# Kernel tuning notes

Measured on AMD Instinct MI355X. Metric: run time of the kernel, lower is better.

The kernel has to match this reference:

```python
import jax, jax.numpy as jnp
import numpy as np

DIM = 256
HEADS = 8
NX = NY = 48
RNG = 5
MAX_IDX = (RNG + 1) ** 2  # 36, padding token


def _make_tokens(nx, ny, rng):
    # Half-symmetric tokenization of 2D relative positions (Learnable_rel_pos_embedding.tokenize)
    xm, ym = np.meshgrid(np.arange(nx), np.arange(ny), indexing='ij')
    xm, ym = xm.ravel(), ym.ravel()
    dx = xm[None, :] - xm[:, None]
    dy = ym[None, :] - ym[:, None]
    tok = np.abs(dx) * (rng + 1) + np.abs(dy)
    tok[(np.abs(dx) > rng) | (np.abs(dy) > rng)] = MAX_IDX
    return tok.astype(np.int32)


def setup_inputs() -> dict:
    key = jax.random.key(0)
    ks = jax.random.split(key, 10)
    s = DIM ** -0.5
    x = jax.random.normal(ks[0], (1, DIM, NX, NY), dtype=jnp.float32)
    Wq = jax.random.normal(ks[1], (DIM, DIM), dtype=jnp.float32) * s
    bq = jax.random.normal(ks[2], (DIM,), dtype=jnp.float32) * 0.01
    Wk = jax.random.normal(ks[3], (DIM, DIM), dtype=jnp.float32) * s
    bk = jax.random.normal(ks[4], (DIM,), dtype=jnp.float32) * 0.01
    Wv = jax.random.normal(ks[5], (DIM, DIM), dtype=jnp.float32) * s
    bv = jax.random.normal(ks[6], (DIM,), dtype=jnp.float32) * 0.01
    Wp = jax.random.normal(ks[7], (DIM, DIM), dtype=jnp.float32) * s
    bp = jax.random.normal(ks[8], (DIM,), dtype=jnp.float32) * 0.01
    emb = jax.random.normal(ks[9], (MAX_IDX + 1, HEADS), dtype=jnp.float32) * 0.02
    tokens = jnp.asarray(_make_tokens(NX, NY, RNG))  # (N, N) int32
    return dict(x=x, Wq=Wq, bq=bq, Wk=Wk, bk=bk, Wv=Wv, bv=bv,
                Wp=Wp, bp=bp, emb=emb, tokens=tokens)


def reference(x, Wq, bq, Wk, bk, Wv, bv, Wp, bp, emb, tokens):
    B, C, nx, ny = x.shape
    H = emb.shape[1]
    hd = C // H
    N = nx * ny
    scale = hd ** -0.5

    def conv1x1(W, b, t):
        return (jnp.einsum('oc,bcxy->boxy', W, t) + b[None, :, None, None])

    # Q/K/V as 1x1 convs, split into heads: (B, H, hd, N)
    q = conv1x1(Wq, bq, x).reshape(B, H, hd, N)
    k = conv1x1(Wk, bk, x).reshape(B, H, hd, N)
    v = conv1x1(Wv, bv, x).reshape(B, H, hd, N)

    # attn_method=2: scores = scale*QK^T + relative positional bias
    scores = jnp.einsum('bhdn,bhdm->bhnm', q, k) * scale  # (B, H, N, N)

    # pos_type=5: embedding lookup over half-symmetric relative-position tokens
    pad = emb.shape[0] - 1
    emb_masked = emb.at[pad].set(0.0)  # padding_idx row is zero
    pe = emb_masked[tokens]            # (N, N, H)
    scores = scores + jnp.transpose(pe, (2, 0, 1))[None]

    attn = jax.nn.softmax(scores, axis=-1)
    out = jnp.einsum('bhnm,bhdm->bhdn', attn, v).reshape(B, C, nx, ny)
    out = conv1x1(Wp, bp, out)
    return out
```

## Files before the change

### kernel.cpp

```cpp
#include <hip/hip_runtime.h>

#define NN 2304
#define CC 256
#define HH 8
#define HD 32
#define NYY 48
#define SCALE 0.17677669529663687f

typedef __bf16 bf16_t;
typedef __bf16 bf8v __attribute__((ext_vector_type(8)));
typedef __bf16 bf4v __attribute__((ext_vector_type(4)));
typedef float f4v __attribute__((ext_vector_type(4)));

__device__ __forceinline__ f4v mfma16(bf8v a, bf8v b, f4v c) {
    return __builtin_amdgcn_mfma_f32_16x16x32_bf16(a, b, c, 0, 0, 0);
}

__global__ __launch_bounds__(256) void k_pre(
    const float* __restrict__ x, bf16_t* __restrict__ xT,
    const float* __restrict__ Wq, const float* __restrict__ Wk,
    const float* __restrict__ Wv, const float* __restrict__ Wp,
    bf16_t* __restrict__ Wb) {
    const int b = blockIdx.x;
    const int t = threadIdx.x;
    if (b < 288) {
        __shared__ float tile[64][33];
        const int c0 = (b & 7) * 32;
        const int n0 = (b >> 3) * 64;
        const int n = t & 63, cb = t >> 6;
#pragma unroll
        for (int cc = 0; cc < 8; cc++) {
            int c = cc * 4 + cb;
            tile[n][c] = x[(size_t)(c0 + c) * NN + n0 + n];
        }
        __syncthreads();
        const int c = t & 31, nb = t >> 5;
#pragma unroll
        for (int nn = 0; nn < 8; nn++) {
            int n2 = nn * 8 + nb;
            xT[(size_t)(n0 + n2) * CC + c0 + c] = (bf16_t)tile[n2][c];
        }
    } else {
        const int wb = b - 288;
        const int matid = wb >> 5;
        const float* src = (matid == 0) ? Wq : (matid == 1) ? Wk : (matid == 2) ? Wv : Wp;
        const int base = (wb & 31) * 2048 + t * 8;
        float4 a = *(const float4*)(src + base);
        float4 c = *(const float4*)(src + base + 4);
        bf8v o;
        o[0] = (bf16_t)a.x; o[1] = (bf16_t)a.y; o[2] = (bf16_t)a.z; o[3] = (bf16_t)a.w;
        o[4] = (bf16_t)c.x; o[5] = (bf16_t)c.y; o[6] = (bf16_t)c.z; o[7] = (bf16_t)c.w;
        *(bf8v*)(Wb + (size_t)matid * 65536 + base) = o;
    }
}

__global__ __launch_bounds__(256) void k_proj_qkv(
    const bf16_t* __restrict__ Wb,
    const float* __restrict__ bq, const float* __restrict__ bk,
    const float* __restrict__ bv,
    const bf16_t* __restrict__ xT,
    bf16_t* __restrict__ Qt, bf16_t* __restrict__ Kt, bf16_t* __restrict__ Vd) {
    const int mat = blockIdx.z;
    const bf16_t* W = Wb + (size_t)mat * 65536;
    const float* bias = (mat == 0) ? bq : (mat == 1) ? bk : bv;
    const int n0 = blockIdx.x * 32;
    const int o0 = blockIdx.y * 64;
    const int lane = threadIdx.x & 63;
    const int wave = threadIdx.x >> 6;
    const int l15 = lane & 15;
    const int quad = lane >> 4;
    const int orow = o0 + wave * 16;

    f4v acc0 = {0.f, 0.f, 0.f, 0.f}, acc1 = {0.f, 0.f, 0.f, 0.f};
#pragma unroll
    for (int k0 = 0; k0 < CC; k0 += 32) {
        bf8v af = *(const bf8v*)(W + (size_t)(orow + l15) * CC + k0 + quad * 8);
        bf8v b0 = *(const bf8v*)(xT + (size_t)(n0 + l15) * CC + k0 + quad * 8);
        bf8v b1 = *(const bf8v*)(xT + (size_t)(n0 + 16 + l15) * CC + k0 + quad * 8);
        acc0 = mfma16(af, b0, acc0);
        acc1 = mfma16(af, b1, acc1);
    }

#pragma unroll
    for (int r = 0; r < 4; r++) {
        const int o = orow + quad * 4 + r;
        const float bo = bias[o];
#pragma unroll
        for (int nb = 0; nb < 2; nb++) {
            const int n = n0 + nb * 16 + l15;
            float v = (nb ? acc1[r] : acc0[r]) + bo;
            if (mat == 2) {
                Vd[(size_t)o * NN + n] = (bf16_t)v;
            } else {
                int h = o >> 5, d = o & 31;
                bf16_t* dst = (mat == 0) ? Qt : Kt;
                float vv = (mat == 0) ? v * SCALE : v;
                dst[(size_t)h * NN * HD + (size_t)n * HD + d] = (bf16_t)vv;
            }
        }
    }
}

template <int NITER, int S>
__global__ __launch_bounds__(256, 6) void k_attn_split(
    const bf16_t* __restrict__ Qt, const bf16_t* __restrict__ Kt,
    const bf16_t* __restrict__ Vd, const float* __restrict__ emb,
    float* __restrict__ pO, float* __restrict__ pl) {
    __shared__ float lds_emb[37];
    const int idx = blockIdx.x;
    const int qt = idx / (8 * S);
    const int rem = idx - qt * (8 * S);
    const int h = rem / S;
    const int sidx = rem - h * S;
    const int t = threadIdx.x;
    if (t < 37) lds_emb[t] = (t < 36) ? __expf(emb[t * HH + h]) : 1.0f;
    __syncthreads();

    const int wave = t >> 6, lane = t & 63;
    const int l15 = lane & 15, quad = lane >> 4;
    const int qg0 = qt * 64 + wave * 16;
    const int q = qg0 + l15;

    const bf16_t* Qh = Qt + (size_t)h * NN * HD;
    const bf16_t* Kh = Kt + (size_t)h * NN * HD;
    const bf16_t* v0p = Vd + (size_t)h * HD * NN + (size_t)l15 * NN;
    const bf16_t* v1p = v0p + (size_t)16 * NN;

    const bf8v aq = *(const bf8v*)(Qh + (size_t)q * HD + quad * 8);
    const int k_begin = sidx * (NITER * 32);

    const int xi = q / NYY, yi = q - (q / NYY) * NYY;
    int kq0 = k_begin + quad * 4;
    int x0 = kq0 / NYY, y0 = kq0 - x0 * NYY;
    int x1 = x0, y1 = y0 + 16;
    if (y1 >= NYY) { y1 -= NYY; x1++; }

    bf8v kf0 = *(const bf8v*)(Kh + (size_t)(k_begin + l15) * HD + quad * 8);
    bf8v kf1 = *(const bf8v*)(Kh + (size_t)(k_begin + 16 + l15) * HD + quad * 8);
    bf4v va0 = *(const bf4v*)(v0p + k_begin + quad * 4);
    bf4v vb0 = *(const bf4v*)(v0p + k_begin + 16 + quad * 4);
    bf4v va1 = *(const bf4v*)(v1p + k_begin + quad * 4);
    bf4v vb1 = *(const bf4v*)(v1p + k_begin + 16 + quad * 4);
    bf8v vf0 = __builtin_shufflevector(va0, vb0, 0, 1, 2, 3, 4, 5, 6, 7);
    bf8v vf1 = __builtin_shufflevector(va1, vb1, 0, 1, 2, 3, 4, 5, 6, 7);

    const f4v z = {0.f, 0.f, 0.f, 0.f};
    f4v o0 = z, o1 = z;
    float lsum = 0.f;

#pragma unroll 1
    for (int it = 0; it < NITER; ++it) {
        const int kb1 = k_begin + ((it + 1 < NITER) ? (it + 1) * 32 : 0);
        bf8v nk0 = *(const bf8v*)(Kh + (size_t)(kb1 + l15) * HD + quad * 8);
        bf8v nk1 = *(const bf8v*)(Kh + (size_t)(kb1 + 16 + l15) * HD + quad * 8);
        bf4v na0 = *(const bf4v*)(v0p + kb1 + quad * 4);
        bf4v nb0 = *(const bf4v*)(v0p + kb1 + 16 + quad * 4);
        bf4v na1 = *(const bf4v*)(v1p + kb1 + quad * 4);
        bf4v nb1 = *(const bf4v*)(v1p + kb1 + 16 + quad * 4);

        f4v s0 = mfma16(kf0, aq, z);
        f4v s1 = mfma16(kf1, aq, z);

        float p[8];
#pragma unroll
        for (int r = 0; r < 4; r++) {
            int yy = y0 + r, xx = x0;
            if (yy >= NYY) { yy -= NYY; xx++; }
            int dy = yi - yy; dy = dy < 0 ? -dy : dy;
            int dx = xi - xx; dx = dx < 0 ? -dx : dx;
            int mx = dx > dy ? dx : dy;
            int tok = mx > 5 ? 36 : dx * 6 + dy;
            p[r] = __expf(s0[r]) * lds_emb[tok];
        }
#pragma unroll
        for (int r = 0; r < 4; r++) {
            int yy = y1 + r, xx = x1;
            if (yy >= NYY) { yy -= NYY; xx++; }
            int dy = yi - yy; dy = dy < 0 ? -dy : dy;
            int dx = xi - xx; dx = dx < 0 ? -dx : dx;
            int mx = dx > dy ? dx : dy;
            int tok = mx > 5 ? 36 : dx * 6 + dy;
            p[4 + r] = __expf(s1[r]) * lds_emb[tok];
        }
#pragma unroll
        for (int j = 0; j < 8; j++) lsum += p[j];
        bf8v pb;
#pragma unroll
        for (int j = 0; j < 8; j++) pb[j] = (bf16_t)p[j];

        o0 = mfma16(vf0, pb, o0);
        o1 = mfma16(vf1, pb, o1);

        kf0 = nk0; kf1 = nk1;
        vf0 = __builtin_shufflevector(na0, nb0, 0, 1, 2, 3, 4, 5, 6, 7);
        vf1 = __builtin_shufflevector(na1, nb1, 0, 1, 2, 3, 4, 5, 6, 7);
        y0 += 32; if (y0 >= NYY) { y0 -= NYY; x0++; }
        y1 += 32; if (y1 >= NYY) { y1 -= NYY; x1++; }
    }

    lsum += __shfl_xor(lsum, 16, 64);
    lsum += __shfl_xor(lsum, 32, 64);

    float* pO_s = pO + ((size_t)sidx * HH + h) * NN * HD;
    *(f4v*)(pO_s + (size_t)q * HD + quad * 4) = o0;
    *(f4v*)(pO_s + (size_t)q * HD + 16 + quad * 4) = o1;
    if (quad == 0) pl[((size_t)sidx * HH + h) * NN + q] = lsum;
}

__global__ __launch_bounds__(256) void k_reduce(
    const float* __restrict__ pO, const float* __restrict__ pl,
    bf16_t* __restrict__ Yt, int S) {
    const int e4 = blockIdx.x * 256 + threadIdx.x;
    const int h = e4 / (NN * HD / 4);
    const int rem = e4 - h * (NN * HD / 4);
    const int q = rem >> 3;
    const int d = (rem & 7) * 4;
    float4 so = {0.f, 0.f, 0.f, 0.f};
    float sl = 0.f;
    for (int s = 0; s < S; s++) {
        const float4 v = *(const float4*)(pO + ((size_t)s * HH + h) * NN * HD + (size_t)q * HD + d);
        so.x += v.x; so.y += v.y; so.z += v.z; so.w += v.w;
        sl += pl[((size_t)s * HH + h) * NN + q];
    }
    const float inv = 1.0f / sl;
    bf4v o;
    o[0] = (bf16_t)(so.x * inv); o[1] = (bf16_t)(so.y * inv);
    o[2] = (bf16_t)(so.z * inv); o[3] = (bf16_t)(so.w * inv);
    *(bf4v*)(Yt + (size_t)q * CC + h * HD + d) = o;
}

__global__ __launch_bounds__(512) void k_proj_out(
    const bf16_t* __restrict__ Wb, const float* __restrict__ bp,
    const bf16_t* __restrict__ Yt, float* __restrict__ out) {
    __shared__ float red[4 * 16 * 32];
    const bf16_t* W = Wb + (size_t)3 * 65536;
    const int n0 = blockIdx.x * 32;
    const int o0 = blockIdx.y * 64;
    const int t = threadIdx.x;
    const int lane = t & 63;
    const int wave = t >> 6;
    const int og = wave & 3;
    const int kg = wave >> 2;
    const int l15 = lane & 15;
    const int quad = lane >> 4;
    const int orow = o0 + og * 16;

    f4v acc0 = {0.f, 0.f, 0.f, 0.f}, acc1 = {0.f, 0.f, 0.f, 0.f};
#pragma unroll
    for (int ki = 0; ki < 4; ki++) {
        const int k0 = kg * 128 + ki * 32;
        bf8v af = *(const bf8v*)(W + (size_t)(orow + l15) * CC + k0 + quad * 8);
        bf8v b0 = *(const bf8v*)(Yt + (size_t)(n0 + l15) * CC + k0 + quad * 8);
        bf8v b1 = *(const bf8v*)(Yt + (size_t)(n0 + 16 + l15) * CC + k0 + quad * 8);
        acc0 = mfma16(af, b0, acc0);
        acc1 = mfma16(af, b1, acc1);
    }

    float* rg = red + og * 512;
    if (kg == 1) {
#pragma unroll
        for (int r = 0; r < 4; r++) {
            rg[(quad * 4 + r) * 32 + l15] = acc0[r];
            rg[(quad * 4 + r) * 32 + 16 + l15] = acc1[r];
        }
    }
    __syncthreads();
    if (kg == 0) {
#pragma unroll
        for (int r = 0; r < 4; r++) {
            const int o = orow + quad * 4 + r;
            const float bo = bp[o];
            out[(size_t)o * NN + n0 + l15] =
                acc0[r] + rg[(quad * 4 + r) * 32 + l15] + bo;
            out[(size_t)o * NN + n0 + 16 + l15] =
                acc1[r] + rg[(quad * 4 + r) * 32 + 16 + l15] + bo;
        }
    }
}

extern "C" void kernel_launch(void* const* d_in, const int* in_sizes, int n_in,
                              void* d_out, int out_size, void* d_ws, size_t ws_size,
                              hipStream_t stream) {
    const float* x   = (const float*)d_in[0];
    const float* Wq  = (const float*)d_in[1];
    const float* bq  = (const float*)d_in[2];
    const float* Wk  = (const float*)d_in[3];
    const float* bk  = (const float*)d_in[4];
    const float* Wv  = (const float*)d_in[5];
    const float* bv  = (const float*)d_in[6];
    const float* Wp  = (const float*)d_in[7];
    const float* bp  = (const float*)d_in[8];
    const float* emb = (const float*)d_in[9];
    float* out = (float*)d_out;

    bf16_t* xT = (bf16_t*)d_ws;
    bf16_t* Qt = xT + (size_t)NN * CC;
    bf16_t* Kt = Qt + (size_t)NN * CC;
    bf16_t* Vd = Kt + (size_t)NN * CC;
    bf16_t* Yt = Vd + (size_t)NN * CC;
    bf16_t* Wb = Yt + (size_t)NN * CC;
    float*  pO = (float*)(Wb + (size_t)4 * CC * CC);

    const size_t base_bytes = (size_t)((char*)pO - (char*)d_ws);
    const size_t per_split = (size_t)HH * NN * HD * 4 + (size_t)HH * NN * 4;
    int S = 1;
    if (base_bytes + 8 * per_split <= ws_size) S = 8;
    else if (base_bytes + 4 * per_split <= ws_size) S = 4;
    else if (base_bytes + 2 * per_split <= ws_size) S = 2;
    float* pl = pO + (size_t)S * HH * NN * HD;

    hipLaunchKernelGGL(k_pre, dim3(416), dim3(256), 0, stream,
                       x, xT, Wq, Wk, Wv, Wp, Wb);
    hipLaunchKernelGGL(k_proj_qkv, dim3(72, 4, 3), dim3(256), 0, stream,
                       Wb, bq, bk, bv, xT, Qt, Kt, Vd);
    switch (S) {
        case 8: hipLaunchKernelGGL((k_attn_split<9, 8>),  dim3(36 * 8 * 8), dim3(256), 0, stream, Qt, Kt, Vd, emb, pO, pl); break;
        case 4: hipLaunchKernelGGL((k_attn_split<18, 4>), dim3(36 * 8 * 4), dim3(256), 0, stream, Qt, Kt, Vd, emb, pO, pl); break;
        case 2: hipLaunchKernelGGL((k_attn_split<36, 2>), dim3(36 * 8 * 2), dim3(256), 0, stream, Qt, Kt, Vd, emb, pO, pl); break;
        default: hipLaunchKernelGGL((k_attn_split<72, 1>), dim3(36 * 8 * 1), dim3(256), 0, stream, Qt, Kt, Vd, emb, pO, pl); break;
    }
    hipLaunchKernelGGL(k_reduce, dim3((HH * NN * HD) / 1024), dim3(256), 0, stream,
                       pO, pl, Yt, S);
    hipLaunchKernelGGL(k_proj_out, dim3(72, 4), dim3(512), 0, stream, Wb, bp, Yt, out);
}
```

Baseline: 166.4 us.

## Skip positional-bias math outside neighbor window, use exp2 and permuted V layout

Folds log2(e) into the Q scale so the attention loop can use exp2f. The per-element relative-position token computation is skipped for key tiles that fall outside the query wave's ±5-row window, where the bias is always exp(0)=1. V is stored in a permuted column order so each lane loads one 8-wide vector instead of two 4-wide ones. Weight bf16 conversion moves out of the pre-kernel into the projection kernels, trading a separate pass for repeated fp32 weight loads and conversions.

New measurement: 157.2 us. 5.5% less time.

```diff
diff --git a/kernel.cpp b/kernel.cpp
--- a/kernel.cpp
+++ b/kernel.cpp
@@ -5,7 +5,7 @@
 #define HH 8
 #define HD 32
 #define NYY 48
-#define SCALE 0.17677669529663687f
+#define QSCALE 0.25503491f
 
 typedef __bf16 bf16_t;
 typedef __bf16 bf8v __attribute__((ext_vector_type(8)));
@@ -16,52 +16,36 @@
     return __builtin_amdgcn_mfma_f32_16x16x32_bf16(a, b, c, 0, 0, 0);
 }
 
-__global__ __launch_bounds__(256) void k_pre(
-    const float* __restrict__ x, bf16_t* __restrict__ xT,
-    const float* __restrict__ Wq, const float* __restrict__ Wk,
-    const float* __restrict__ Wv, const float* __restrict__ Wp,
-    bf16_t* __restrict__ Wb) {
+__global__ __launch_bounds__(256) void k_pre(const float* __restrict__ x,
+                                             bf16_t* __restrict__ xT) {
+    __shared__ float tile[64][33];
     const int b = blockIdx.x;
     const int t = threadIdx.x;
-    if (b < 288) {
-        __shared__ float tile[64][33];
-        const int c0 = (b & 7) * 32;
-        const int n0 = (b >> 3) * 64;
-        const int n = t & 63, cb = t >> 6;
-#pragma unroll
-        for (int cc = 0; cc < 8; cc++) {
-            int c = cc * 4 + cb;
-            tile[n][c] = x[(size_t)(c0 + c) * NN + n0 + n];
-        }
-        __syncthreads();
-        const int c = t & 31, nb = t >> 5;
-#pragma unroll
-        for (int nn = 0; nn < 8; nn++) {
-            int n2 = nn * 8 + nb;
-            xT[(size_t)(n0 + n2) * CC + c0 + c] = (bf16_t)tile[n2][c];
-        }
-    } else {
-        const int wb = b - 288;
-        const int matid = wb >> 5;
-        const float* src = (matid == 0) ? Wq : (matid == 1) ? Wk : (matid == 2) ? Wv : Wp;
-        const int base = (wb & 31) * 2048 + t * 8;
-        float4 a = *(const float4*)(src + base);
-        float4 c = *(const float4*)(src + base + 4);
-        bf8v o;
-        o[0] = (bf16_t)a.x; o[1] = (bf16_t)a.y; o[2] = (bf16_t)a.z; o[3] = (bf16_t)a.w;
-        o[4] = (bf16_t)c.x; o[5] = (bf16_t)c.y; o[6] = (bf16_t)c.z; o[7] = (bf16_t)c.w;
-        *(bf8v*)(Wb + (size_t)matid * 65536 + base) = o;
+    const int c0 = (b & 7) * 32;
+    const int n0 = (b >> 3) * 64;
+    const int n = t & 63, cb = t >> 6;
+#pragma unroll
+    for (int cc = 0; cc < 8; cc++) {
+        int c = cc * 4 + cb;
+        tile[n][c] = x[(size_t)(c0 + c) * NN + n0 + n];
+    }
+    __syncthreads();
+    const int c = t & 31, nb = t >> 5;
+#pragma unroll
+    for (int nn = 0; nn < 8; nn++) {
+        int n2 = nn * 8 + nb;
+        xT[(size_t)(n0 + n2) * CC + c0 + c] = (bf16_t)tile[n2][c];
     }
 }
 
 __global__ __launch_bounds__(256) void k_proj_qkv(
-    const bf16_t* __restrict__ Wb,
-    const float* __restrict__ bq, const float* __restrict__ bk,
-    const float* __restrict__ bv,
+    const float* __restrict__ Wq, const float* __restrict__ bq,
+    const float* __restrict__ Wk, const float* __restrict__ bk,
+    const float* __restrict__ Wv, const float* __restrict__ bv,
     const bf16_t* __restrict__ xT,
     bf16_t* __restrict__ Qt, bf16_t* __restrict__ Kt, bf16_t* __restrict__ Vd) {
     const int mat = blockIdx.z;
-    const bf16_t* W = Wb + (size_t)mat * 65536;
+    const float* W = (mat == 0) ? Wq : (mat == 1) ? Wk : Wv;
     const float* bias = (mat == 0) ? bq : (mat == 1) ? bk : bv;
     const int n0 = blockIdx.x * 32;
     const int o0 = blockIdx.y * 64;
@@ -74,7 +58,14 @@
     f4v acc0 = {0.f, 0.f, 0.f, 0.f}, acc1 = {0.f, 0.f, 0.f, 0.f};
 #pragma unroll
     for (int k0 = 0; k0 < CC; k0 += 32) {
-        bf8v af = *(const bf8v*)(W + (size_t)(orow + l15) * CC + k0 + quad * 8);
+        const float* wp = W + (size_t)(orow + l15) * CC + k0 + quad * 8;
+        float4 wa = *(const float4*)wp;
+        float4 wc = *(const float4*)(wp + 4);
+        bf8v af;
+        af[0] = (bf16_t)wa.x; af[1] = (bf16_t)wa.y;
+        af[2] = (bf16_t)wa.z; af[3] = (bf16_t)wa.w;
+        af[4] = (bf16_t)wc.x; af[5] = (bf16_t)wc.y;
+        af[6] = (bf16_t)wc.z; af[7] = (bf16_t)wc.w;
         bf8v b0 = *(const bf8v*)(xT + (size_t)(n0 + l15) * CC + k0 + quad * 8);
         bf8v b1 = *(const bf8v*)(xT + (size_t)(n0 + 16 + l15) * CC + k0 + quad * 8);
         acc0 = mfma16(af, b0, acc0);
@@ -90,11 +81,12 @@
             const int n = n0 + nb * 16 + l15;
             float v = (nb ? acc1[r] : acc0[r]) + bo;
             if (mat == 2) {
-                Vd[(size_t)o * NN + n] = (bf16_t)v;
+                int pos = (l15 >> 2) * 8 + (l15 & 3) + 4 * nb;
+                Vd[(size_t)o * NN + n0 + pos] = (bf16_t)v;
             } else {
                 int h = o >> 5, d = o & 31;
                 bf16_t* dst = (mat == 0) ? Qt : Kt;
-                float vv = (mat == 0) ? v * SCALE : v;
+                float vv = (mat == 0) ? v * QSCALE : v;
                 dst[(size_t)h * NN * HD + (size_t)n * HD + d] = (bf16_t)vv;
             }
         }
@@ -120,6 +112,12 @@
     const int l15 = lane & 15, quad = lane >> 4;
     const int qg0 = qt * 64 + wave * 16;
     const int q = qg0 + l15;
+    const int xi = q / NYY, yi = q - xi * NYY;
+
+    const int qg0u = __builtin_amdgcn_readfirstlane(qg0);
+    const int xlo = qg0u / NYY, xhi = (qg0u + 15) / NYY;
+    const int klo = (xlo - 5) * NYY;
+    const int khi = (xhi + 5) * NYY + NYY - 1;
 
     const bf16_t* Qh = Qt + (size_t)h * NN * HD;
     const bf16_t* Kh = Kt + (size_t)h * NN * HD;
@@ -129,34 +127,29 @@
     const bf8v aq = *(const bf8v*)(Qh + (size_t)q * HD + quad * 8);
     const int k_begin = sidx * (NITER * 32);
 
-    const int xi = q / NYY, yi = q - (q / NYY) * NYY;
-    int kq0 = k_begin + quad * 4;
-    int x0 = kq0 / NYY, y0 = kq0 - x0 * NYY;
-    int x1 = x0, y1 = y0 + 16;
-    if (y1 >= NYY) { y1 -= NYY; x1++; }
-
-    bf8v kf0 = *(const bf8v*)(Kh + (size_t)(k_begin + l15) * HD + quad * 8);
-    bf8v kf1 = *(const bf8v*)(Kh + (size_t)(k_begin + 16 + l15) * HD + quad * 8);
-    bf4v va0 = *(const bf4v*)(v0p + k_begin + quad * 4);
-    bf4v vb0 = *(const bf4v*)(v0p + k_begin + 16 + quad * 4);
-    bf4v va1 = *(const bf4v*)(v1p + k_begin + quad * 4);
-    bf4v vb1 = *(const bf4v*)(v1p + k_begin + 16 + quad * 4);
-    bf8v vf0 = __builtin_shufflevector(va0, vb0, 0, 1, 2, 3, 4, 5, 6, 7);
-    bf8v vf1 = __builtin_shufflevector(va1, vb1, 0, 1, 2, 3, 4, 5, 6, 7);
+    const bf16_t* kp0 = Kh + (size_t)(k_begin + l15) * HD + quad * 8;
+    const bf16_t* kp1 = kp0 + 16 * HD;
+    const bf16_t* vp0 = v0p + k_begin + quad * 8;
+    const bf16_t* vp1 = v1p + k_begin + quad * 8;
+
+    bf8v kf0 = *(const bf8v*)kp0;
+    bf8v kf1 = *(const bf8v*)kp1;
+    bf8v vf0 = *(const bf8v*)vp0;
+    bf8v vf1 = *(const bf8v*)vp1;
+    kp0 += 32 * HD; kp1 += 32 * HD; vp0 += 32; vp1 += 32;
 
     const f4v z = {0.f, 0.f, 0.f, 0.f};
     f4v o0 = z, o1 = z;
     float lsum = 0.f;
+    int kb = k_begin;
 
 #pragma unroll 1
     for (int it = 0; it < NITER; ++it) {
-        const int kb1 = k_begin + ((it + 1 < NITER) ? (it + 1) * 32 : 0);
-        bf8v nk0 = *(const bf8v*)(Kh + (size_t)(kb1 + l15) * HD + quad * 8);
-        bf8v nk1 = *(const bf8v*)(Kh + (size_t)(kb1 + 16 + l15) * HD + quad * 8);
-        bf4v na0 = *(const bf4v*)(v0p + kb1 + quad * 4);
-        bf4v nb0 = *(const bf4v*)(v0p + kb1 + 16 + quad * 4);
-        bf4v na1 = *(const bf4v*)(v1p + kb1 + quad * 4);
-        bf4v nb1 = *(const bf4v*)(v1p + kb1 + 16 + quad * 4);
+        bf8v nk0 = *(const bf8v*)kp0;
+        bf8v nk1 = *(const bf8v*)kp1;
+        bf8v nv0 = *(const bf8v*)vp0;
+        bf8v nv1 = *(const bf8v*)vp1;
+        kp0 += 32 * HD; kp1 += 32 * HD; vp0 += 32; vp1 += 32;
 
         f4v s0 = mfma16(kf0, aq, z);
         f4v s1 = mfma16(kf1, aq, z);
@@ -164,24 +157,35 @@
         float p[8];
 #pragma unroll
         for (int r = 0; r < 4; r++) {
-            int yy = y0 + r, xx = x0;
-            if (yy >= NYY) { yy -= NYY; xx++; }
-            int dy = yi - yy; dy = dy < 0 ? -dy : dy;
-            int dx = xi - xx; dx = dx < 0 ? -dx : dx;
-            int mx = dx > dy ? dx : dy;
-            int tok = mx > 5 ? 36 : dx * 6 + dy;
-            p[r] = __expf(s0[r]) * lds_emb[tok];
-        }
-#pragma unroll
-        for (int r = 0; r < 4; r++) {
-            int yy = y1 + r, xx = x1;
-            if (yy >= NYY) { yy -= NYY; xx++; }
-            int dy = yi - yy; dy = dy < 0 ? -dy : dy;
-            int dx = xi - xx; dx = dx < 0 ? -dx : dx;
-            int mx = dx > dy ? dx : dy;
-            int tok = mx > 5 ? 36 : dx * 6 + dy;
-            p[4 + r] = __expf(s1[r]) * lds_emb[tok];
-        }
+            p[r] = exp2f(s0[r]);
+            p[4 + r] = exp2f(s1[r]);
+        }
+
+        if (kb + 31 >= klo && kb <= khi) {
+            const int kqa = kb + quad * 4;
+            const int xa = kqa / NYY, ya = kqa - xa * NYY;
+            const int kqb = kqa + 16;
+            const int xb = kqb / NYY, yb = kqb - xb * NYY;
+#pragma unroll
+            for (int r = 0; r < 4; r++) {
+                int yy = ya + r, xx = xa;
+                if (yy >= NYY) { yy -= NYY; xx++; }
+                int dy = yi - yy; dy = dy < 0 ? -dy : dy;
+                int dx = xi - xx; dx = dx < 0 ? -dx : dx;
+                int tok = (dx > 5 || dy > 5) ? 36 : dx * 6 + dy;
+                p[r] *= lds_emb[tok];
+            }
+#pragma unroll
+            for (int r = 0; r < 4; r++) {
+                int yy = yb + r, xx = xb;
+                if (yy >= NYY) { yy -= NYY; xx++; }
+                int dy = yi - yy; dy = dy < 0 ? -dy : dy;
+                int dx = xi - xx; dx = dx < 0 ? -dx : dx;
+                int tok = (dx > 5 || dy > 5) ? 36 : dx * 6 + dy;
+                p[4 + r] *= lds_emb[tok];
+            }
+        }
+
 #pragma unroll
         for (int j = 0; j < 8; j++) lsum += p[j];
         bf8v pb;
@@ -191,11 +195,8 @@
         o0 = mfma16(vf0, pb, o0);
         o1 = mfma16(vf1, pb, o1);
 
-        kf0 = nk0; kf1 = nk1;
-        vf0 = __builtin_shufflevector(na0, nb0, 0, 1, 2, 3, 4, 5, 6, 7);
-        vf1 = __builtin_shufflevector(na1, nb1, 0, 1, 2, 3, 4, 5, 6, 7);
-        y0 += 32; if (y0 >= NYY) { y0 -= NYY; x0++; }
-        y1 += 32; if (y1 >= NYY) { y1 -= NYY; x1++; }
+        kf0 = nk0; kf1 = nk1; vf0 = nv0; vf1 = nv1;
+        kb += 32;
     }
 
     lsum += __shfl_xor(lsum, 16, 64);
@@ -230,10 +231,9 @@
 }
 
 __global__ __launch_bounds__(512) void k_proj_out(
-    const bf16_t* __restrict__ Wb, const float* __restrict__ bp,
+    const float* __restrict__ Wp, const float* __restrict__ bp,
     const bf16_t* __restrict__ Yt, float* __restrict__ out) {
     __shared__ float red[4 * 16 * 32];
-    const bf16_t* W = Wb + (size_t)3 * 65536;
     const int n0 = blockIdx.x * 32;
     const int o0 = blockIdx.y * 64;
     const int t = threadIdx.x;
@@ -249,7 +249,14 @@
 #pragma unroll
     for (int ki = 0; ki < 4; ki++) {
         const int k0 = kg * 128 + ki * 32;
-        bf8v af = *(const bf8v*)(W + (size_t)(orow + l15) * CC + k0 + quad * 8);
+        const float* wp = Wp + (size_t)(orow + l15) * CC + k0 + quad * 8;
+        float4 wa = *(const float4*)wp;
+        float4 wc = *(const float4*)(wp + 4);
+        bf8v af;
+        af[0] = (bf16_t)wa.x; af[1] = (bf16_t)wa.y;
+        af[2] = (bf16_t)wa.z; af[3] = (bf16_t)wa.w;
+        af[4] = (bf16_t)wc.x; af[5] = (bf16_t)wc.y;
+        af[6] = (bf16_t)wc.z; af[7] = (bf16_t)wc.w;
         bf8v b0 = *(const bf8v*)(Yt + (size_t)(n0 + l15) * CC + k0 + quad * 8);
         bf8v b1 = *(const bf8v*)(Yt + (size_t)(n0 + 16 + l15) * CC + k0 + quad * 8);
         acc0 = mfma16(af, b0, acc0);
@@ -298,8 +305,7 @@
     bf16_t* Kt = Qt + (size_t)NN * CC;
     bf16_t* Vd = Kt + (size_t)NN * CC;
     bf16_t* Yt = Vd + (size_t)NN * CC;
-    bf16_t* Wb = Yt + (size_t)NN * CC;
-    float*  pO = (float*)(Wb + (size_t)4 * CC * CC);
+    float*  pO = (float*)(Yt + (size_t)NN * CC);
 
     const size_t base_bytes = (size_t)((char*)pO - (char*)d_ws);
     const size_t per_split = (size_t)HH * NN * HD * 4 + (size_t)HH * NN * 4;
@@ -309,10 +315,9 @@
     else if (base_bytes + 2 * per_split <= ws_size) S = 2;
     float* pl = pO + (size_t)S * HH * NN * HD;
 
-    hipLaunchKernelGGL(k_pre, dim3(416), dim3(256), 0, stream,
-                       x, xT, Wq, Wk, Wv, Wp, Wb);
+    hipLaunchKernelGGL(k_pre, dim3(288), dim3(256), 0, stream, x, xT);
     hipLaunchKernelGGL(k_proj_qkv, dim3(72, 4, 3), dim3(256), 0, stream,
-                       Wb, bq, bk, bv, xT, Qt, Kt, Vd);
+                       Wq, bq, Wk, bk, Wv, bv, xT, Qt, Kt, Vd);
     switch (S) {
         case 8: hipLaunchKernelGGL((k_attn_split<9, 8>),  dim3(36 * 8 * 8), dim3(256), 0, stream, Qt, Kt, Vd, emb, pO, pl); break;
         case 4: hipLaunchKernelGGL((k_attn_split<18, 4>), dim3(36 * 8 * 4), dim3(256), 0, stream, Qt, Kt, Vd, emb, pO, pl); break;
@@ -321,5 +326,5 @@
     }
     hipLaunchKernelGGL(k_reduce, dim3((HH * NN * HD) / 1024), dim3(256), 0, stream,
                        pO, pl, Yt, S);
-    hipLaunchKernelGGL(k_proj_out, dim3(72, 4), dim3(512), 0, stream, Wb, bp, Yt, out);
-}
+    hipLaunchKernelGGL(k_proj_out, dim3(72, 4), dim3(512), 0, stream, Wp, bp, Yt, out);
+}
```
